# Kernel optimization log

Measured on AMD Instinct MI355X. Metric: run time of the kernel, lower is better.

## Reference

```python
import jax, jax.numpy as jnp
import numpy as np
import string

N_QUBITS = 16
N_LAYERS = 2
BATCH = 32
DIM = 2 ** N_QUBITS


def _apply_1q(psi, U, q):
    # psi: (B,) + (2,)*n complex; U: (2,2) complex acting on qubit q
    n = psi.ndim - 1
    ax = string.ascii_lowercase[:n]
    out = list(ax)
    out[q] = 'A'
    return jnp.einsum('A' + ax[q] + ',z' + ax + '->z' + ''.join(out), U, psi)


def _apply_2q(psi, G, c, t):
    # G: (2,2,2,2) = (out_c, out_t, in_c, in_t)
    n = psi.ndim - 1
    ax = string.ascii_lowercase[:n]
    out = list(ax)
    out[c] = 'A'
    out[t] = 'B'
    return jnp.einsum('AB' + ax[c] + ax[t] + ',z' + ax + '->z' + ''.join(out), G, psi)


def _rx(th):
    c = jnp.cos(th * 0.5).astype(jnp.complex64)
    s = jnp.sin(th * 0.5).astype(jnp.complex64)
    return jnp.array([[c, -1j * s], [-1j * s, c]])


def _ry(th):
    c = jnp.cos(th * 0.5).astype(jnp.complex64)
    s = jnp.sin(th * 0.5).astype(jnp.complex64)
    return jnp.array([[c, -s], [s, c]])


def _rz(th):
    th_c = th.astype(jnp.complex64)
    z = jnp.zeros((), jnp.complex64)
    return jnp.array([[jnp.exp(-0.5j * th_c), z], [z, jnp.exp(0.5j * th_c)]])


_CNOT = jnp.array([[1, 0, 0, 0],
                   [0, 1, 0, 0],
                   [0, 0, 0, 1],
                   [0, 0, 1, 0]], dtype=jnp.complex64).reshape(2, 2, 2, 2)


def setup_inputs() -> dict:
    key = jax.random.key(0)
    k1, k2, k3 = jax.random.split(key, 3)
    thetas = jax.random.normal(k1, (N_LAYERS, 3, N_QUBITS), dtype=jnp.float32)
    re = jax.random.normal(k2, (BATCH, DIM), dtype=jnp.float32)
    im = jax.random.normal(k3, (BATCH, DIM), dtype=jnp.float32)
    norm = jnp.sqrt(jnp.sum(re * re + im * im, axis=-1, keepdims=True))
    return {"thetas": thetas, "state_re": re / norm, "state_im": im / norm}


def reference(thetas, state_re, state_im):
    B = state_re.shape[0]
    psi = (state_re.astype(jnp.complex64) + 1j * state_im.astype(jnp.complex64))
    psi = psi.reshape((B,) + (2,) * N_QUBITS)
    for l in range(N_LAYERS):
        for q in range(N_QUBITS):
            psi = _apply_1q(psi, _rx(thetas[l, 0, q]), q)
            psi = _apply_1q(psi, _ry(thetas[l, 1, q]), q)
            psi = _apply_1q(psi, _rz(thetas[l, 2, q]), q)
        for q in range(N_QUBITS):
            psi = _apply_2q(psi, _CNOT, q, (q + 1) % N_QUBITS)
    probs = (psi.real ** 2 + psi.imag ** 2).reshape(B, -1)
    return probs
```

## Files before the change

kernel.cpp:

```cpp
#include <hip/hip_runtime.h>


#define NT 512

__device__ __forceinline__ int fperm(int x) {
  int y = x ^ (x >> 1);
  y ^= (x & 1) ? 0xC000 : 0;
  return y & 0xFFFF;
}

__device__ __forceinline__ int finv16(int x) {
  int s = x;
  s ^= s >> 1; s ^= s >> 2; s ^= s >> 4; s ^= s >> 8;
  int b15 = ((s ^ (s >> 15)) & 1) << 15;
  return (s & 0x7FFF) | b15;
}

__device__ __forceinline__ int swz(int l) { return l ^ ((l >> 4) & 31); }

__global__ void gates_k(const float* __restrict__ th, float* __restrict__ gbuf) {
  int tid = threadIdx.x;
  if (tid < 32) {
    int l = tid >> 4, q = tid & 15;
    float tx = th[l * 48 + q], ty = th[l * 48 + 16 + q], tz = th[l * 48 + 32 + q];
    float cx, sx, cy, sy, cz, sz;
    sincosf(0.5f * tx, &sx, &cx);
    sincosf(0.5f * ty, &sy, &cy);
    sincosf(0.5f * tz, &sz, &cz);
    float m00r = cy * cx, m00i =  sy * sx;
    float m01r = -sy * cx, m01i = -cy * sx;
    float m10r =  sy * cx, m10i = -cy * sx;
    float m11r =  cy * cx, m11i = -sy * sx;
    float* G = gbuf + tid * 8;
    G[0] = cz * m00r + sz * m00i;  G[1] = cz * m00i - sz * m00r;
    G[2] = cz * m01r + sz * m01i;  G[3] = cz * m01i - sz * m01r;
    G[4] = cz * m10r - sz * m10i;  G[5] = cz * m10i + sz * m10r;
    G[6] = cz * m11r - sz * m11i;  G[7] = cz * m11i + sz * m11r;
  }
}

template <int MK, int SK>
__device__ __forceinline__ void greg(float (&ar)[16], float (&ai)[16],
                                     const float* __restrict__ G, int c) {
  const float4* G4 = (const float4*)G;
  float4 r0 = G4[0], r1 = G4[1];
  bool sw = (c != 0);
  float h00r = sw ? r1.z : r0.x, h00i = sw ? r1.w : r0.y;
  float h01r = sw ? r1.x : r0.z, h01i = sw ? r1.y : r0.w;
  float h10r = sw ? r0.z : r1.x, h10i = sw ? r0.w : r1.y;
  float h11r = sw ? r0.x : r1.z, h11i = sw ? r0.y : r1.w;
  constexpr int PV = MK & (-MK);
#pragma unroll
  for (int k = 0; k < 16; k++) {
    if (k & PV) continue;
    const int k2 = k ^ MK;
    const int p0 = __builtin_popcount(k & SK) & 1;
    const int ka = p0 ? k2 : k;
    const int kb = p0 ? k : k2;
    float xr = ar[ka], xi = ai[ka], yr = ar[kb], yi = ai[kb];
    ar[ka] = h00r * xr - h00i * xi + h01r * yr - h01i * yi;
    ai[ka] = h00r * xi + h00i * xr + h01r * yi + h01i * yr;
    ar[kb] = h10r * xr - h10i * xi + h11r * yr - h11i * yi;
    ai[kb] = h10r * xi + h10i * xr + h11r * yi + h11i * yr;
  }
}

__global__ void __launch_bounds__(NT) pass1_k(const float* __restrict__ gbuf,
                                              const float* __restrict__ xre,
                                              const float* __restrict__ xim,
                                              float2* __restrict__ ws) {
  __shared__ float sre[8192], sim[8192];
  int t = threadIdx.x;
  int blk = blockIdx.x, batch = blk >> 3, hi3 = blk & 7;
  int base = batch * 65536 + (hi3 << 13);
  float ar[16], ai[16];

  {
    const float4* xr4 = (const float4*)(xre + base + (t << 4));
    const float4* xi4 = (const float4*)(xim + base + (t << 4));
#pragma unroll
    for (int q = 0; q < 4; q++) {
      float4 v = xr4[q]; ar[4*q] = v.x; ar[4*q+1] = v.y; ar[4*q+2] = v.z; ar[4*q+3] = v.w;
      float4 w = xi4[q]; ai[4*q] = w.x; ai[4*q+1] = w.y; ai[4*q+2] = w.z; ai[4*q+3] = w.w;
    }
    greg<1, 1>(ar, ai, gbuf + 15 * 8, 0);
    greg<2, 2>(ar, ai, gbuf + 14 * 8, 0);
    greg<4, 4>(ar, ai, gbuf + 13 * 8, 0);
    greg<8, 8>(ar, ai, gbuf + 12 * 8, 0);
#pragma unroll
    for (int k = 0; k < 16; k++) { int s = swz((t << 4) | k); sre[s] = ar[k]; sim[s] = ai[k]; }
  }
  __syncthreads();
  {
#pragma unroll
    for (int k = 0; k < 16; k++) {
      int s = swz((t & 15) | (k << 4) | ((t >> 4) << 8));
      ar[k] = sre[s]; ai[k] = sim[s];
    }
    greg<1, 1>(ar, ai, gbuf + 11 * 8, 0);
    greg<2, 2>(ar, ai, gbuf + 10 * 8, 0);
    greg<4, 4>(ar, ai, gbuf + 9 * 8, 0);
    greg<8, 8>(ar, ai, gbuf + 8 * 8, 0);
#pragma unroll
    for (int k = 0; k < 16; k++) {
      int s = swz((t & 15) | (k << 4) | ((t >> 4) << 8));
      sre[s] = ar[k]; sim[s] = ai[k];
    }
  }
  __syncthreads();
  {
#pragma unroll
    for (int k = 0; k < 16; k++) {
      int s = swz((t & 255) | (k << 8) | ((t >> 8) << 12));
      ar[k] = sre[s]; ai[k] = sim[s];
    }
    greg<1, 1>(ar, ai, gbuf + 7 * 8, 0);
    greg<2, 2>(ar, ai, gbuf + 6 * 8, 0);
    greg<4, 4>(ar, ai, gbuf + 5 * 8, 0);
    greg<8, 8>(ar, ai, gbuf + 4 * 8, 0);
#pragma unroll
    for (int k = 0; k < 16; k++) {
      int s = swz((t & 255) | (k << 8) | ((t >> 8) << 12));
      sre[s] = ar[k]; sim[s] = ai[k];
    }
  }
  __syncthreads();
  {
#pragma unroll
    for (int k = 0; k < 16; k++) {
      int s = swz((k & 7) | (t << 3) | ((k >> 3) << 12));
      ar[k] = sre[s]; ai[k] = sim[s];
    }
    greg<8, 8>(ar, ai, gbuf + 3 * 8, 0);
#pragma unroll
    for (int k = 0; k < 16; k += 2) {
      float4* p = (float4*)(ws + base + (k & 7) + (t << 3) + ((k >> 3) << 12));
      *p = make_float4(ar[k], ai[k], ar[k + 1], ai[k + 1]);
    }
  }
}

__global__ void __launch_bounds__(NT) pass2_k(const float* __restrict__ gbuf,
                                              float2* __restrict__ ws) {
  __shared__ float sre[8192], sim[8192];
  int t = threadIdx.x;
  int blk = blockIdx.x, batch = blk >> 3, mid3 = blk & 7;
  int bbase = batch * 65536, mb = mid3 << 10;
  float ar[16], ai[16];

  {
#pragma unroll
    for (int k = 0; k < 16; k += 2) {
      int f2 = (k & 1) | (t << 1) | mb | ((k >> 1) << 13);
      float4 v = *(const float4*)(ws + bbase + f2);
      ar[k] = v.x; ai[k] = v.y; ar[k + 1] = v.z; ai[k + 1] = v.w;
    }
    int fbase = (t << 1) | mb;
    int codd = __popc(fbase) & 1;
    greg<2, 2>(ar, ai, gbuf + 2 * 8, 0);
    greg<4, 4>(ar, ai, gbuf + 1 * 8, 0);
    greg<8, 8>(ar, ai, gbuf + 0 * 8, 0);
    greg<12, 7>(ar, ai, gbuf + (16 + 0) * 8, codd);
    greg<6, 12>(ar, ai, gbuf + (16 + 1) * 8, 0);
    greg<13, 15>(ar, ai, gbuf + (16 + 15) * 8, codd);
#pragma unroll
    for (int k = 0; k < 16; k++) {
      int s = swz((k & 1) | (t << 1) | ((k >> 1) << 10));
      sre[s] = ar[k]; sim[s] = ai[k];
    }
  }
  __syncthreads();
  {
#pragma unroll
    for (int k = 0; k < 16; k++) {
      int s = swz(k | (t << 4)); ar[k] = sre[s]; ai[k] = sim[s];
    }
    int lA = t << 4;
    int fbase = (lA & 1023) | mb | ((lA >> 10) << 13);
    int c = __popc(fbase) & 1;
    greg<3, 14>(ar, ai, gbuf + (16 + 14) * 8, c);
    greg<6, 12>(ar, ai, gbuf + (16 + 13) * 8, c);
    greg<12, 8>(ar, ai, gbuf + (16 + 12) * 8, c);
#pragma unroll
    for (int k = 0; k < 16; k++) {
      int s = swz(k | (t << 4)); sre[s] = ar[k]; sim[s] = ai[k];
    }
  }
  __syncthreads();
  {
#pragma unroll
    for (int k = 0; k < 16; k++) {
      int s = swz((t & 7) | (k << 3) | ((t >> 3) << 7));
      ar[k] = sre[s]; ai[k] = sim[s];
    }
    int lA = (t & 7) | ((t >> 3) << 7);
    int fbase = (lA & 1023) | mb | ((lA >> 10) << 13);
    int c = __popc(fbase & 0xFFF0) & 1;
    greg<3, 14>(ar, ai, gbuf + (16 + 11) * 8, c);
    greg<6, 12>(ar, ai, gbuf + (16 + 10) * 8, c);
    greg<12, 8>(ar, ai, gbuf + (16 + 9) * 8, c);
#pragma unroll
    for (int k = 0; k < 16; k++) {
      int s = swz((t & 7) | (k << 3) | ((t >> 3) << 7));
      sre[s] = ar[k]; sim[s] = ai[k];
    }
  }
  __syncthreads();
  {
#pragma unroll
    for (int k = 0; k < 16; k++) {
      int s = swz((t & 63) | (k << 6) | ((t >> 6) << 10));
      ar[k] = sre[s]; ai[k] = sim[s];
    }
    int lA = (t & 63) | ((t >> 6) << 10);
    int fbase = (lA & 1023) | mb | ((lA >> 10) << 13);
    int c = __popc(fbase & 0xFF80) & 1;
    greg<3, 14>(ar, ai, gbuf + (16 + 8) * 8, c);
    greg<6, 12>(ar, ai, gbuf + (16 + 7) * 8, c);
    greg<12, 8>(ar, ai, gbuf + (16 + 6) * 8, c);
#pragma unroll
    for (int k = 0; k < 16; k++) {
      int f2 = (t & 63) | (k << 6) | mb | ((t >> 6) << 13);
      ws[bbase + f2] = make_float2(ar[k], ai[k]);
    }
  }
}

__global__ void __launch_bounds__(NT) pass3_k(const float* __restrict__ gbuf,
                                              const float2* __restrict__ ws,
                                              float* __restrict__ out) {
  int t = threadIdx.x;
  int blk = blockIdx.x, batch = blk >> 3, g3 = blk & 7;
  int bbase = batch * 65536;
  int gb = ((g3 & 1) << 9) | ((g3 >> 1) << 14);
  int jt = (t & 0x1FF) | gb;
  float ar[16], ai[16];
#pragma unroll
  for (int k = 0; k < 16; k++) {
    int j = jt | (k << 10);
    float2 v = ws[bbase + fperm(j)];
    ar[k] = v.x; ai[k] = v.y;
  }
  greg<1, 1>(ar, ai, gbuf + (16 + 5) * 8, 0);
  greg<2, 2>(ar, ai, gbuf + (16 + 4) * 8, 0);
  greg<4, 4>(ar, ai, gbuf + (16 + 3) * 8, 0);
  greg<8, 8>(ar, ai, gbuf + (16 + 2) * 8, 0);
#pragma unroll
  for (int k = 0; k < 16; k++) {
    int j = jt | (k << 10);
    out[bbase + finv16(j)] = ar[k] * ar[k] + ai[k] * ai[k];
  }
}

extern "C" void kernel_launch(void* const* d_in, const int* in_sizes, int n_in,
                              void* d_out, int out_size, void* d_ws, size_t ws_size,
                              hipStream_t stream) {
  const float* th  = (const float*)d_in[0];
  const float* xre = (const float*)d_in[1];
  const float* xim = (const float*)d_in[2];
  float* out = (float*)d_out;

  float* gbuf = (float*)d_ws;
  float2* amp = (float2*)((float*)d_ws + 256);

  gates_k<<<1, 64, 0, stream>>>(th, gbuf);
  pass1_k<<<256, NT, 0, stream>>>(gbuf, xre, xim, amp);
  pass2_k<<<256, NT, 0, stream>>>(gbuf, amp);
  pass3_k<<<256, NT, 0, stream>>>(gbuf, amp, out);
}
```

Measured before the change: 108.8 us.

## Fuse gate computation into passes and repartition qubits across smaller blocks

Drops the separate gate-matrix kernel; each pass recomputes the gate matrices into shared memory, which removes one launch and the global dependency on it. The work is repartitioned into 256-thread blocks covering 4096 amplitudes, giving 512 blocks per pass instead of 256 and halving shared memory per block. Pass1 now applies 12 gates and pass2 picks up the remaining Rx/Ry/Rz gates along with more CNOTs. Pass3 handles 32 amplitudes per thread across 5 qubits. The trade-off is redundant sincos work in every block and different global access patterns, with some non-vectorised float2 stores.

Measured after the change: 104.2 us. -4.2%, faster.

```diff
diff --git a/kernel.cpp b/kernel.cpp
--- a/kernel.cpp
+++ b/kernel.cpp
@@ -1,7 +1,7 @@
 #include <hip/hip_runtime.h>
 
 
-#define NT 512
+#define NT 256
 
 __device__ __forceinline__ int fperm(int x) {
   int y = x ^ (x >> 1);
@@ -16,9 +16,10 @@
   return (s & 0x7FFF) | b15;
 }
 
-__device__ __forceinline__ int swz(int l) { return l ^ ((l >> 4) & 31); }
-
-__global__ void gates_k(const float* __restrict__ th, float* __restrict__ gbuf) {
+__device__ __forceinline__ int swz1(int l) { return l ^ ((l >> 4) & 31); }
+__device__ __forceinline__ int swz2(int l) { return l ^ ((l >> 5) & 31); }
+
+__device__ __forceinline__ void compute_gates(const float* __restrict__ th, float* gsh) {
   int tid = threadIdx.x;
   if (tid < 32) {
     int l = tid >> 4, q = tid & 15;
@@ -31,7 +32,7 @@
     float m01r = -sy * cx, m01i = -cy * sx;
     float m10r =  sy * cx, m10i = -cy * sx;
     float m11r =  cy * cx, m11i = -sy * sx;
-    float* G = gbuf + tid * 8;
+    float* G = gsh + tid * 8;
     G[0] = cz * m00r + sz * m00i;  G[1] = cz * m00i - sz * m00r;
     G[2] = cz * m01r + sz * m01i;  G[3] = cz * m01i - sz * m01r;
     G[4] = cz * m10r - sz * m10i;  G[5] = cz * m10i + sz * m10r;
@@ -39,9 +40,9 @@
   }
 }
 
-template <int MK, int SK>
-__device__ __forceinline__ void greg(float (&ar)[16], float (&ai)[16],
-                                     const float* __restrict__ G, int c) {
+template <int MK, int SK, int N>
+__device__ __forceinline__ void greg(float (&ar)[N], float (&ai)[N],
+                                     const float* G, int c) {
   const float4* G4 = (const float4*)G;
   float4 r0 = G4[0], r1 = G4[1];
   bool sw = (c != 0);
@@ -51,7 +52,7 @@
   float h11r = sw ? r0.x : r1.z, h11i = sw ? r0.y : r1.w;
   constexpr int PV = MK & (-MK);
 #pragma unroll
-  for (int k = 0; k < 16; k++) {
+  for (int k = 0; k < N; k++) {
     if (k & PV) continue;
     const int k2 = k ^ MK;
     const int p0 = __builtin_popcount(k & SK) & 1;
@@ -65,16 +66,18 @@
   }
 }
 
-__global__ void __launch_bounds__(NT) pass1_k(const float* __restrict__ gbuf,
+__global__ void __launch_bounds__(NT) pass1_k(const float* __restrict__ th,
                                               const float* __restrict__ xre,
                                               const float* __restrict__ xim,
                                               float2* __restrict__ ws) {
-  __shared__ float sre[8192], sim[8192];
+  __shared__ float gsh[256];
+  __shared__ float sre[4096], sim[4096];
   int t = threadIdx.x;
-  int blk = blockIdx.x, batch = blk >> 3, hi3 = blk & 7;
-  int base = batch * 65536 + (hi3 << 13);
+  int blk = blockIdx.x, batch = blk >> 4, wb = blk & 15;
+  int base = batch * 65536 + (wb << 12);
   float ar[16], ai[16];
 
+  compute_gates(th, gsh);
   {
     const float4* xr4 = (const float4*)(xre + base + (t << 4));
     const float4* xi4 = (const float4*)(xim + base + (t << 4));
@@ -83,171 +86,145 @@
       float4 v = xr4[q]; ar[4*q] = v.x; ar[4*q+1] = v.y; ar[4*q+2] = v.z; ar[4*q+3] = v.w;
       float4 w = xi4[q]; ai[4*q] = w.x; ai[4*q+1] = w.y; ai[4*q+2] = w.z; ai[4*q+3] = w.w;
     }
-    greg<1, 1>(ar, ai, gbuf + 15 * 8, 0);
-    greg<2, 2>(ar, ai, gbuf + 14 * 8, 0);
-    greg<4, 4>(ar, ai, gbuf + 13 * 8, 0);
-    greg<8, 8>(ar, ai, gbuf + 12 * 8, 0);
-#pragma unroll
-    for (int k = 0; k < 16; k++) { int s = swz((t << 4) | k); sre[s] = ar[k]; sim[s] = ai[k]; }
-  }
-  __syncthreads();
+  }
+  __syncthreads();
+  greg<1, 1>(ar, ai, gsh + 15 * 8, 0);
+  greg<2, 2>(ar, ai, gsh + 14 * 8, 0);
+  greg<4, 4>(ar, ai, gsh + 13 * 8, 0);
+  greg<8, 8>(ar, ai, gsh + 12 * 8, 0);
+#pragma unroll
+  for (int k = 0; k < 16; k++) { int s = swz1((t << 4) | k); sre[s] = ar[k]; sim[s] = ai[k]; }
+  __syncthreads();
+#pragma unroll
+  for (int k = 0; k < 16; k++) {
+    int s = swz1((t & 15) | (k << 4) | ((t >> 4) << 8));
+    ar[k] = sre[s]; ai[k] = sim[s];
+  }
+  greg<1, 1>(ar, ai, gsh + 11 * 8, 0);
+  greg<2, 2>(ar, ai, gsh + 10 * 8, 0);
+  greg<4, 4>(ar, ai, gsh + 9 * 8, 0);
+  greg<8, 8>(ar, ai, gsh + 8 * 8, 0);
+#pragma unroll
+  for (int k = 0; k < 16; k++) {
+    int s = swz1((t & 15) | (k << 4) | ((t >> 4) << 8));
+    sre[s] = ar[k]; sim[s] = ai[k];
+  }
+  __syncthreads();
+#pragma unroll
+  for (int k = 0; k < 16; k++) {
+    int s = swz1(t | (k << 8)); ar[k] = sre[s]; ai[k] = sim[s];
+  }
+  greg<1, 1>(ar, ai, gsh + 7 * 8, 0);
+  greg<2, 2>(ar, ai, gsh + 6 * 8, 0);
+  greg<4, 4>(ar, ai, gsh + 5 * 8, 0);
+  greg<8, 8>(ar, ai, gsh + 4 * 8, 0);
+#pragma unroll
+  for (int k = 0; k < 16; k++)
+    ws[base + t + (k << 8)] = make_float2(ar[k], ai[k]);
+}
+
+__global__ void __launch_bounds__(NT) pass2_k(const float* __restrict__ th,
+                                              float2* __restrict__ ws) {
+  __shared__ float gsh[256];
+  __shared__ float sre[4096], sim[4096];
+  int t = threadIdx.x;
+  int blk = blockIdx.x, batch = blk >> 4, wb = blk & 15;
+  int bbase = batch * 65536;
+  float ar[16], ai[16];
+
+  compute_gates(th, gsh);
+#pragma unroll
+  for (int k = 0; k < 16; k++) {
+    float2 v = ws[bbase + t + (wb << 8) + (k << 12)];
+    ar[k] = v.x; ai[k] = v.y;
+  }
+  __syncthreads();
+  int cA = (__popc(t) + __popc(wb)) & 1;
+  greg<1, 1>(ar, ai, gsh + 3 * 8, 0);
+  greg<2, 2>(ar, ai, gsh + 2 * 8, 0);
+  greg<4, 4>(ar, ai, gsh + 1 * 8, 0);
+  greg<8, 8>(ar, ai, gsh + 0 * 8, 0);
+  greg<12, 7>(ar, ai, gsh + (16 + 0) * 8, cA);
+  greg<6, 12>(ar, ai, gsh + (16 + 1) * 8, 0);
+  greg<3, 14>(ar, ai, gsh + (16 + 2) * 8, 0);
+#pragma unroll
+  for (int k = 0; k < 16; k++) {
+    int s = swz2(t | (k << 8)); sre[s] = ar[k]; sim[s] = ai[k];
+  }
+  __syncthreads();
+#pragma unroll
+  for (int k = 0; k < 16; k++) {
+    int s = swz2((k & 3) | (t << 2) | ((k >> 2) << 10));
+    ar[k] = sre[s]; ai[k] = sim[s];
+  }
+  greg<13, 15>(ar, ai, gsh + (16 + 15) * 8, cA);
+  greg<3, 14>(ar, ai, gsh + (16 + 14) * 8, cA);
+#pragma unroll
+  for (int k = 0; k < 16; k++) {
+    int s = swz2((k & 3) | (t << 2) | ((k >> 2) << 10));
+    sre[s] = ar[k]; sim[s] = ai[k];
+  }
+  __syncthreads();
+#pragma unroll
+  for (int k = 0; k < 16; k++) {
+    int s = swz2((t & 1) | (k << 1) | ((t >> 1) << 5));
+    ar[k] = sre[s]; ai[k] = sim[s];
+  }
   {
-#pragma unroll
-    for (int k = 0; k < 16; k++) {
-      int s = swz((t & 15) | (k << 4) | ((t >> 4) << 8));
-      ar[k] = sre[s]; ai[k] = sim[s];
-    }
-    greg<1, 1>(ar, ai, gbuf + 11 * 8, 0);
-    greg<2, 2>(ar, ai, gbuf + 10 * 8, 0);
-    greg<4, 4>(ar, ai, gbuf + 9 * 8, 0);
-    greg<8, 8>(ar, ai, gbuf + 8 * 8, 0);
-#pragma unroll
-    for (int k = 0; k < 16; k++) {
-      int s = swz((t & 15) | (k << 4) | ((t >> 4) << 8));
-      sre[s] = ar[k]; sim[s] = ai[k];
-    }
-  }
-  __syncthreads();
+    int cC = (__popc(t >> 1) + __popc(wb)) & 1;
+    greg<3, 14>(ar, ai, gsh + (16 + 13) * 8, cC);
+    greg<6, 12>(ar, ai, gsh + (16 + 12) * 8, cC);
+    greg<12, 8>(ar, ai, gsh + (16 + 11) * 8, cC);
+  }
+#pragma unroll
+  for (int k = 0; k < 16; k++) {
+    int s = swz2((t & 1) | (k << 1) | ((t >> 1) << 5));
+    sre[s] = ar[k]; sim[s] = ai[k];
+  }
+  __syncthreads();
+#pragma unroll
+  for (int k = 0; k < 16; k++) {
+    int s = swz2((t & 15) | (k << 4) | ((t >> 4) << 8));
+    ar[k] = sre[s]; ai[k] = sim[s];
+  }
   {
-#pragma unroll
-    for (int k = 0; k < 16; k++) {
-      int s = swz((t & 255) | (k << 8) | ((t >> 8) << 12));
-      ar[k] = sre[s]; ai[k] = sim[s];
-    }
-    greg<1, 1>(ar, ai, gbuf + 7 * 8, 0);
-    greg<2, 2>(ar, ai, gbuf + 6 * 8, 0);
-    greg<4, 4>(ar, ai, gbuf + 5 * 8, 0);
-    greg<8, 8>(ar, ai, gbuf + 4 * 8, 0);
-#pragma unroll
-    for (int k = 0; k < 16; k++) {
-      int s = swz((t & 255) | (k << 8) | ((t >> 8) << 12));
-      sre[s] = ar[k]; sim[s] = ai[k];
-    }
-  }
-  __syncthreads();
-  {
-#pragma unroll
-    for (int k = 0; k < 16; k++) {
-      int s = swz((k & 7) | (t << 3) | ((k >> 3) << 12));
-      ar[k] = sre[s]; ai[k] = sim[s];
-    }
-    greg<8, 8>(ar, ai, gbuf + 3 * 8, 0);
-#pragma unroll
-    for (int k = 0; k < 16; k += 2) {
-      float4* p = (float4*)(ws + base + (k & 7) + (t << 3) + ((k >> 3) << 12));
-      *p = make_float4(ar[k], ai[k], ar[k + 1], ai[k + 1]);
-    }
-  }
-}
-
-__global__ void __launch_bounds__(NT) pass2_k(const float* __restrict__ gbuf,
-                                              float2* __restrict__ ws) {
-  __shared__ float sre[8192], sim[8192];
-  int t = threadIdx.x;
-  int blk = blockIdx.x, batch = blk >> 3, mid3 = blk & 7;
-  int bbase = batch * 65536, mb = mid3 << 10;
-  float ar[16], ai[16];
-
-  {
-#pragma unroll
-    for (int k = 0; k < 16; k += 2) {
-      int f2 = (k & 1) | (t << 1) | mb | ((k >> 1) << 13);
-      float4 v = *(const float4*)(ws + bbase + f2);
-      ar[k] = v.x; ai[k] = v.y; ar[k + 1] = v.z; ai[k + 1] = v.w;
-    }
-    int fbase = (t << 1) | mb;
-    int codd = __popc(fbase) & 1;
-    greg<2, 2>(ar, ai, gbuf + 2 * 8, 0);
-    greg<4, 4>(ar, ai, gbuf + 1 * 8, 0);
-    greg<8, 8>(ar, ai, gbuf + 0 * 8, 0);
-    greg<12, 7>(ar, ai, gbuf + (16 + 0) * 8, codd);
-    greg<6, 12>(ar, ai, gbuf + (16 + 1) * 8, 0);
-    greg<13, 15>(ar, ai, gbuf + (16 + 15) * 8, codd);
-#pragma unroll
-    for (int k = 0; k < 16; k++) {
-      int s = swz((k & 1) | (t << 1) | ((k >> 1) << 10));
-      sre[s] = ar[k]; sim[s] = ai[k];
-    }
-  }
-  __syncthreads();
-  {
-#pragma unroll
-    for (int k = 0; k < 16; k++) {
-      int s = swz(k | (t << 4)); ar[k] = sre[s]; ai[k] = sim[s];
-    }
-    int lA = t << 4;
-    int fbase = (lA & 1023) | mb | ((lA >> 10) << 13);
-    int c = __popc(fbase) & 1;
-    greg<3, 14>(ar, ai, gbuf + (16 + 14) * 8, c);
-    greg<6, 12>(ar, ai, gbuf + (16 + 13) * 8, c);
-    greg<12, 8>(ar, ai, gbuf + (16 + 12) * 8, c);
-#pragma unroll
-    for (int k = 0; k < 16; k++) {
-      int s = swz(k | (t << 4)); sre[s] = ar[k]; sim[s] = ai[k];
-    }
-  }
-  __syncthreads();
-  {
-#pragma unroll
-    for (int k = 0; k < 16; k++) {
-      int s = swz((t & 7) | (k << 3) | ((t >> 3) << 7));
-      ar[k] = sre[s]; ai[k] = sim[s];
-    }
-    int lA = (t & 7) | ((t >> 3) << 7);
-    int fbase = (lA & 1023) | mb | ((lA >> 10) << 13);
-    int c = __popc(fbase & 0xFFF0) & 1;
-    greg<3, 14>(ar, ai, gbuf + (16 + 11) * 8, c);
-    greg<6, 12>(ar, ai, gbuf + (16 + 10) * 8, c);
-    greg<12, 8>(ar, ai, gbuf + (16 + 9) * 8, c);
-#pragma unroll
-    for (int k = 0; k < 16; k++) {
-      int s = swz((t & 7) | (k << 3) | ((t >> 3) << 7));
-      sre[s] = ar[k]; sim[s] = ai[k];
-    }
-  }
-  __syncthreads();
-  {
-#pragma unroll
-    for (int k = 0; k < 16; k++) {
-      int s = swz((t & 63) | (k << 6) | ((t >> 6) << 10));
-      ar[k] = sre[s]; ai[k] = sim[s];
-    }
-    int lA = (t & 63) | ((t >> 6) << 10);
-    int fbase = (lA & 1023) | mb | ((lA >> 10) << 13);
-    int c = __popc(fbase & 0xFF80) & 1;
-    greg<3, 14>(ar, ai, gbuf + (16 + 8) * 8, c);
-    greg<6, 12>(ar, ai, gbuf + (16 + 7) * 8, c);
-    greg<12, 8>(ar, ai, gbuf + (16 + 6) * 8, c);
-#pragma unroll
-    for (int k = 0; k < 16; k++) {
-      int f2 = (t & 63) | (k << 6) | mb | ((t >> 6) << 13);
-      ws[bbase + f2] = make_float2(ar[k], ai[k]);
-    }
-  }
-}
-
-__global__ void __launch_bounds__(NT) pass3_k(const float* __restrict__ gbuf,
+    int cD = (__popc(t >> 4) + __popc(wb)) & 1;
+    greg<3, 14>(ar, ai, gsh + (16 + 10) * 8, cD);
+    greg<6, 12>(ar, ai, gsh + (16 + 9) * 8, cD);
+    greg<12, 8>(ar, ai, gsh + (16 + 8) * 8, cD);
+  }
+#pragma unroll
+  for (int k = 0; k < 16; k++) {
+    int full = (t & 15) | (k << 4) | (wb << 8) | ((t >> 4) << 12);
+    ws[bbase + full] = make_float2(ar[k], ai[k]);
+  }
+}
+
+__global__ void __launch_bounds__(NT) pass3_k(const float* __restrict__ th,
                                               const float2* __restrict__ ws,
                                               float* __restrict__ out) {
+  __shared__ float gsh[256];
   int t = threadIdx.x;
   int blk = blockIdx.x, batch = blk >> 3, g3 = blk & 7;
   int bbase = batch * 65536;
-  int gb = ((g3 & 1) << 9) | ((g3 >> 1) << 14);
-  int jt = (t & 0x1FF) | gb;
-  float ar[16], ai[16];
-#pragma unroll
-  for (int k = 0; k < 16; k++) {
-    int j = jt | (k << 10);
+  int jt = t | (g3 << 13);
+  float ar[32], ai[32];
+  compute_gates(th, gsh);
+#pragma unroll
+  for (int k = 0; k < 32; k++) {
+    int j = jt | (k << 8);
     float2 v = ws[bbase + fperm(j)];
     ar[k] = v.x; ai[k] = v.y;
   }
-  greg<1, 1>(ar, ai, gbuf + (16 + 5) * 8, 0);
-  greg<2, 2>(ar, ai, gbuf + (16 + 4) * 8, 0);
-  greg<4, 4>(ar, ai, gbuf + (16 + 3) * 8, 0);
-  greg<8, 8>(ar, ai, gbuf + (16 + 2) * 8, 0);
-#pragma unroll
-  for (int k = 0; k < 16; k++) {
-    int j = jt | (k << 10);
+  __syncthreads();
+  greg<1, 1>(ar, ai, gsh + (16 + 7) * 8, 0);
+  greg<2, 2>(ar, ai, gsh + (16 + 6) * 8, 0);
+  greg<4, 4>(ar, ai, gsh + (16 + 5) * 8, 0);
+  greg<8, 8>(ar, ai, gsh + (16 + 4) * 8, 0);
+  greg<16, 16>(ar, ai, gsh + (16 + 3) * 8, 0);
+#pragma unroll
+  for (int k = 0; k < 32; k++) {
+    int j = jt | (k << 8);
     out[bbase + finv16(j)] = ar[k] * ar[k] + ai[k] * ai[k];
   }
 }
@@ -260,11 +237,9 @@
   const float* xim = (const float*)d_in[2];
   float* out = (float*)d_out;
 
-  float* gbuf = (float*)d_ws;
-  float2* amp = (float2*)((float*)d_ws + 256);
-
-  gates_k<<<1, 64, 0, stream>>>(th, gbuf);
-  pass1_k<<<256, NT, 0, stream>>>(gbuf, xre, xim, amp);
-  pass2_k<<<256, NT, 0, stream>>>(gbuf, amp);
-  pass3_k<<<256, NT, 0, stream>>>(gbuf, amp, out);
-}
+  float2* amp = (float2*)d_ws;
+
+  pass1_k<<<512, NT, 0, stream>>>(th, xre, xim, amp);
+  pass2_k<<<512, NT, 0, stream>>>(th, amp);
+  pass3_k<<<256, NT, 0, stream>>>(th, amp, out);
+}
```
